# Kernel optimization log

Measured on AMD Instinct MI355X. Metric: run time of the kernel, lower is better.

The kernel has to match this reference:

```python
import jax, jax.numpy as jnp
import numpy as np

P_SIZE = 13
B_THRESH = 1.3  # |u| >= b -> hard 1.0
N_POW = 64      # u^n / (u^n + 1)


def make_dct_weight(p):
    idx = np.arange(p)
    Ci = np.where(idx == 0, 1.0 / np.sqrt(2.0), 1.0)
    cos = np.cos((2 * idx[:, None] + 1) * idx[None, :] * np.pi / (2 * p)) * Ci[None, :]  # [x,i]
    P = (2.0 / p) * np.einsum('xi,yj->xyij', cos, cos).reshape(p * p, p * p)
    return P.T.astype(np.float32).reshape(p * p, 1, p, p)


def conv2d(x, w, padding):
    return jax.lax.conv_general_dilated(x, w, (1, 1), padding,
                                        dimension_numbers=('NCHW', 'OIHW', 'NCHW'))


def udiff(u):
    # x^64/(x^64+1), saturated to 1 for |x| >= 1.3 (even power, sign-safe)
    au = jnp.abs(u)
    us = jnp.where(au < B_THRESH, u, 0.0)  # avoid overflow in pow
    y = us ** N_POW
    return jnp.where(au >= B_THRESH, jnp.ones_like(u), y / (y + 1.0))


def setup_inputs() -> dict:
    key = jax.random.key(0)
    k1, _ = jax.random.split(key)
    x = jax.random.uniform(k1, (2, 1, 512, 512), dtype=jnp.float32)
    sigma = jnp.full((1,), 0.1, dtype=jnp.float32)
    W_dct = jnp.asarray(make_dct_weight(P_SIZE))  # [p^2, 1, p, p], learnable in original
    return {"x": x, "sigma": sigma, "W_dct": W_dct}


def reference(x, sigma, W_dct):
    N, _, H, W = x.shape
    p = W_dct.shape[-1]
    pp = p * p
    # patch DCT: [N, p^2, H-p+1, W-p+1]
    t = conv2d(x, W_dct, 'VALID')
    nz = udiff(t / (3.0 * sigma))
    y = t * nz
    w = 1.0 / (1.0 + jnp.sum(nz, axis=1, keepdims=True))  # [N,1,H',W']
    # inverse transform as 1x1 conv with inv(dct matrix)
    Minv = jnp.linalg.inv(W_dct.reshape(pp, pp))
    z = jnp.einsum('kc,nchw->nkhw', Minv, y)
    z = w * z
    # overlap-add fold == conv with spatially-flipped identity patch kernel, full padding
    fold_k = jnp.flip(jnp.eye(pp, dtype=x.dtype).reshape(pp, p, p), axis=(1, 2))[None]  # [1,p^2,p,p]
    folded = conv2d(z, fold_k, [(p - 1, p - 1), (p - 1, p - 1)])  # [N,1,H,W]
    out = folded[:, :, p - 1:H - (p - 1), p - 1:W - (p - 1)]
    divisor = conv2d(w, jnp.ones((1, 1, p, p), x.dtype), 'VALID')
    return out / divisor
```

## Files before the change

### kernel.cpp

```cpp
#include <hip/hip_runtime.h>
#include <math.h>


#define P13    13
#define IMGW   512
#define OUTW   488
#define SEGH   31
#define NSEG   16
#define HCOLS  512
#define HPITCH 16

struct C1mat { float v[P13 * P13]; };

constexpr double kPI = 3.14159265358979323846264338327950288;

constexpr double ccos_pm_pi(double th) {
    double term = 1.0, s = 1.0;
    const double th2 = th * th;
    for (int n = 1; n <= 25; ++n) {
        term *= -th2 / (double)((2 * n - 1) * (2 * n));
        s += term;
    }
    return s;
}
constexpr double csqrt(double v) {
    double x = (v > 1.0) ? v : 1.0;
    for (int i = 0; i < 64; ++i) x = 0.5 * (x + v / x);
    return x;
}
constexpr C1mat make_c1() {
    C1mat m{};
    const double s213 = csqrt(2.0 / 13.0);
    const double is2  = 1.0 / csqrt(2.0);
    for (int x = 0; x < P13; ++x)
        for (int k = 0; k < P13; ++k) {
            int mm = ((2 * x + 1) * k) % 52;
            double th = (mm <= 26) ? (mm * kPI / 26.0) : ((mm - 52) * kPI / 26.0);
            double Ci = (k == 0) ? is2 : 1.0;
            m.v[x * P13 + k] = (float)(s213 * Ci * ccos_pm_pi(th));
        }
    return m;
}
__device__ constexpr C1mat c1c = make_c1();

struct CTab { int idx[P13][P13]; bool neg[P13][P13]; float a[14]; float b[6]; };
constexpr CTab make_ctab() {
    CTab t{};
    const double s213 = csqrt(2.0 / 13.0);
    for (int q = 0; q <= 12; ++q) t.a[q] = (float)(s213 * ccos_pm_pi(q * kPI / 26.0));
    t.a[13] = (float)(s213 / csqrt(2.0));
    for (int q = 0; q < 6; ++q) t.b[q] = (float)(2.0 * ccos_pm_pi((q + 1) * kPI / 13.0));
    for (int r = 0; r < P13; ++r)
        for (int c = 0; c < P13; ++c) {
            if (c == 0) { t.idx[r][c] = 13; t.neg[r][c] = false; continue; }
            int m = ((2 * r + 1) * c) % 52;
            int q; bool n;
            if (m <= 13)      { q = m;      n = false; }
            else if (m <= 26) { q = 26 - m; n = true;  }
            else if (m <= 39) { q = m - 26; n = true;  }
            else              { q = 52 - m; n = false; }
            t.idx[r][c] = q; t.neg[r][c] = n;
        }
    return t;
}
constexpr CTab ctab = make_ctab();

#define KC(r, c) (ctab.neg[(r)][(c)] ? -As[ctab.idx[(r)][(c)]] : As[ctab.idx[(r)][(c)]])

struct FalseT { static constexpr bool value = false; };
struct TrueT  { static constexpr bool value = true; };

#define ROR16_ADD(v, N)                                                        \
    v += __int_as_float(__builtin_amdgcn_mov_dpp(__float_as_int(v),            \
                                                 0x120 + (N), 0xF, 0xF, true))

__device__ __forceinline__ void fold_vert(const float (&tn)[P13], const float (&As)[14],
                                          float w1, float (&H)[P13])
{
#pragma unroll
    for (int dx = 0; dx < 6; ++dx) {
        float E = KC(dx, 0) * tn[0];
#pragma unroll
        for (int i = 2; i < P13; i += 2) E = fmaf(KC(dx, i), tn[i], E);
        float O = KC(dx, 1) * tn[1];
#pragma unroll
        for (int i = 3; i < P13; i += 2) O = fmaf(KC(dx, i), tn[i], O);
        H[dx]      = fmaf(w1, E + O, H[dx]);
        H[12 - dx] = fmaf(w1, E - O, H[12 - dx]);
    }
    float z6 = KC(6, 0) * tn[0];
#pragma unroll
    for (int i = 2; i < P13; i += 2) z6 = fmaf(KC(6, i), tn[i], z6);
    H[6] = fmaf(w1, z6, H[6]);
}

__global__ __launch_bounds__(256) void dct2net_k2(
    const float* __restrict__ xg, const float* __restrict__ sigmag,
    float* __restrict__ Hg, float* __restrict__ Wg)
{
    __shared__ float c1lds[169];
    const int tid = threadIdx.x;
    if (tid < 169) c1lds[tid] = c1c.v[tid];
    __syncthreads();

    const int lane = tid & 63;
    const int wv   = tid >> 6;
    const int g    = lane >> 4;
    const int jj   = lane & 15;
    const int img  = blockIdx.z;
    const int hs   = blockIdx.y * SEGH;
    const int segrows = (OUTW - hs < SEGH) ? (OUTW - hs) : SEGH;
    const int cbw  = blockIdx.x * 16 + wv * 4;
    const int col  = cbw + g;

    const float inv3s = 1.0f / (3.0f * sigmag[0]);
    const float* xin  = xg + (size_t)img * IMGW * IMGW;

    float As[14], Bs[6];
#pragma unroll
    for (int q = 0; q < 14; ++q) As[q] = ctab.a[q];
#pragma unroll
    for (int q = 0; q < 6; ++q) Bs[q] = ctab.b[q];
#pragma unroll
    for (int q = 0; q < 14; ++q) asm("" : "+s"(As[q]));
#pragma unroll
    for (int q = 0; q < 6; ++q) asm("" : "+s"(Bs[q]));

    float c1col[P13];
#pragma unroll
    for (int y = 0; y < P13; ++y)
        c1col[y] = (jj < 13) ? c1lds[y * P13 + jj] * inv3s : 0.0f;

    float T0[P13], T1[P13], dr[P13], Hr[P13], wr[12], Rv[P13];
#pragma unroll
    for (int k = 0; k < P13; ++k) { T0[k]=0; T1[k]=0; dr[k]=0; Hr[k]=0; Rv[k]=0; }
#pragma unroll
    for (int k = 0; k < 12; ++k) wr[k] = 0.0f;
    float vs = 0.0f, Rprev = 0.0f;

    int xcol = cbw + (lane & 15); xcol = (xcol < IMGW - 1) ? xcol : (IMGW - 1);
    const float* xp    = xin + (size_t)hs * IMGW;
    const float* xlast = xin + (size_t)(IMGW - 1) * IMGW;
    float xv = xp[xcol];
    xp += IMGW;

    float* Hp = Hg + ((size_t)img * OUTW + hs) * HCOLS * HPITCH;
    float* Wp = Wg + ((size_t)img * IMGW + hs) * IMGW;
    const int voH = col * HPITCH + jj;
    const int voW = col;

    auto front = [&]() -> float {
        float xw[P13];
#pragma unroll
        for (int y = 0; y < P13; ++y)
            xw[y] = __int_as_float(
                __builtin_amdgcn_ds_bpermute(4 * (g + y), __float_as_int(xv)));
        { const float* xq = (xp < xlast) ? xp : xlast; xv = xq[xcol]; xp += IMGW; }
        float a0 = c1col[0] * xw[0], a1 = c1col[1] * xw[1];
#pragma unroll
        for (int y = 2; y < P13; y += 2) a0 = fmaf(c1col[y], xw[y], a0);
#pragma unroll
        for (int y = 3; y < P13; y += 2) a1 = fmaf(c1col[y], xw[y], a1);
        return a0 + a1;
    };
    auto pushRv = [&](float Rn) {
#pragma unroll
        for (int q = 0; q < P13 - 1; ++q) Rv[q] = Rv[q + 1];
        Rv[P13 - 1] = Rn;
    };
    auto pushd = [&](float Rn) {
        float dn = Rn - Rprev; Rprev = Rn;
#pragma unroll
        for (int q = 0; q < P13 - 1; ++q) dr[q] = dr[q + 1];
        dr[P13 - 1] = dn;
    };
    auto matvec = [&](float (&T)[P13]) {
        float Se[6], So[6];
#pragma unroll
        for (int k = 0; k < 6; ++k) { Se[k] = Rv[k] + Rv[12 - k]; So[k] = Rv[k] - Rv[12 - k]; }
#pragma unroll
        for (int i = 0; i < P13; ++i) {
            float t;
            if ((i & 1) == 0) {
                t = KC(6, i) * Rv[6];
#pragma unroll
                for (int k = 0; k < 6; ++k) t = fmaf(KC(k, i), Se[k], t);
            } else {
                t = KC(0, i) * So[0];
#pragma unroll
                for (int k = 1; k < 6; ++k) t = fmaf(KC(k, i), So[k], t);
            }
            T[i] = t;
        }
    };
    auto sf = [&](const float (&T)[P13], bool rt) {
        float tn[P13]; float pnzr = 0.0f;
#pragma unroll
        for (int i = 0; i < P13; ++i) {
            float p2 = fminf(T[i] * T[i], 1.69f);
            float p4 = p2 * p2, p8 = p4 * p4, p16 = p8 * p8, p32 = p16 * p16, p64 = p32 * p32;
            float r  = __builtin_amdgcn_rcpf(p64 + 1.0f);
            pnzr += r;
            tn[i] = fmaf(-T[i], r, T[i]);
        }
        float pnz = 13.0f - pnzr;
        ROR16_ADD(pnz, 1); ROR16_ADD(pnz, 2); ROR16_ADD(pnz, 4); ROR16_ADD(pnz, 8);
        const float w = __builtin_amdgcn_rcpf(1.0f + pnz);
        vs += w;
        fold_vert(tn, As, w, Hr);
        if (rt) {
            Hp[voH] = Hr[0];
            Hp += HCOLS * HPITCH;
            if (jj == 0) Wp[voW] = vs;
            Wp += IMGW;
            vs -= wr[0];
        }
#pragma unroll
        for (int q = 0; q < 11; ++q) wr[q] = wr[q + 1];
        wr[11] = w;
#pragma unroll
        for (int q = 0; q < P13 - 1; ++q) Hr[q] = Hr[q + 1];
        Hr[P13 - 1] = 0.0f;
    };
    auto recur = [&](auto INTOT0, bool rt) {
        float Rn = front();
        float dn = Rn - Rprev; Rprev = Rn;
        float dl = dr[0];
#pragma unroll
        for (int q = 0; q < P13 - 1; ++q) dr[q] = dr[q + 1];
        dr[P13 - 1] = dn;
        float Pe = dn - dl, Po = dn + dl;
#pragma unroll
        for (int i = 0; i < P13; ++i) {
            float tp2 = decltype(INTOT0)::value ? T0[i] : T1[i];
            float tp1 = decltype(INTOT0)::value ? T1[i] : T0[i];
            float c2 = (i == 0) ? 2.0f : ((i <= 6) ? Bs[i - 1] : -Bs[12 - i]);
            float t = fmaf(c2, tp1, -tp2);
            float kc = (i == 0) ? As[13] : As[i];
            t = (i & 1) ? fmaf(-kc, Po, t) : fmaf(kc, Pe, t);
            if constexpr (decltype(INTOT0)::value) T0[i] = t; else T1[i] = t;
        }
        if constexpr (decltype(INTOT0)::value) sf(T0, rt); else sf(T1, rt);
    };

    { float Rn = front(); Rprev = Rn; pushRv(Rn); }
#pragma unroll 1
    for (int k = 1; k < 12; ++k) { float Rn = front(); pushd(Rn); pushRv(Rn); }
    { float Rn = front(); pushd(Rn); pushRv(Rn); matvec(T0); sf(T0, false); }
    { float Rn = front(); pushd(Rn); pushRv(Rn); matvec(T1); sf(T1, false); }
    {
        int ks = 0; const int S = 10 + segrows;
#pragma unroll 1
        while (ks + 2 <= S) {
            recur(TrueT{},  ks     >= 10);
            recur(FalseT{}, ks + 1 >= 10);
            ks += 2;
        }
        if (ks < S) recur(TrueT{}, ks >= 10);
    }
}

__global__ __launch_bounds__(256) void dct2net_k3(
    const float* __restrict__ Hg, const float* __restrict__ Wg,
    const float* __restrict__ sigmag, float* __restrict__ outg)
{
    __shared__ float U[4][76][14];
    __shared__ float vw[4][80];
    const int tid  = threadIdx.x;
    const int lane = tid & 63;
    const int wv   = tid >> 6;
    const int img  = blockIdx.z;
    const int a0   = blockIdx.y * 4;
    const int a    = a0 + wv;
    const int cb   = blockIdx.x * 64;

    const float t3s = 3.0f * sigmag[0];

    float As[14];
#pragma unroll
    for (int q = 0; q < 14; ++q) As[q] = ctab.a[q];
#pragma unroll
    for (int q = 0; q < 14; ++q) asm("" : "+s"(As[q]));

    int c = cb + lane; c = (c < 499) ? c : 499;
    const float* hp = &Hg[(((size_t)img * OUTW + a) * HCOLS + c) * HPITCH];
    float4 m0 = *(const float4*)hp;
    float4 m1 = *(const float4*)(hp + 4);
    float4 m2 = *(const float4*)(hp + 8);
    float  m3 = hp[12];
    float  wm = Wg[((size_t)img * IMGW + a) * IMGW + c];

    const bool halo = (tid < 48);
    const int  hr = tid / 12;
    const int  hm = tid - hr * 12;
    float4 s0 = {0,0,0,0}, s1 = {0,0,0,0}, s2 = {0,0,0,0};
    float  s3 = 0.0f, ws = 0.0f;
    if (halo) {
        const int ah = a0 + hr;
        int c2 = cb + 64 + hm; c2 = (c2 < 499) ? c2 : 499;
        const float* hq = &Hg[(((size_t)img * OUTW + ah) * HCOLS + c2) * HPITCH];
        s0 = *(const float4*)hq;
        s1 = *(const float4*)(hq + 4);
        s2 = *(const float4*)(hq + 8);
        s3 = hq[12];
        ws = Wg[((size_t)img * IMGW + ah) * IMGW + c2];
    }

    auto buildU = [&](const float (&hv)[P13], int uw, int uli) {
#pragma unroll
        for (int dy = 0; dy < 6; ++dy) {
            float e = KC(dy, 0) * hv[0];
#pragma unroll
            for (int j = 2; j < P13; j += 2) e = fmaf(KC(dy, j), hv[j], e);
            float o = KC(dy, 1) * hv[1];
#pragma unroll
            for (int j = 3; j < P13; j += 2) o = fmaf(KC(dy, j), hv[j], o);
            U[uw][uli][dy]      = e + o;
            U[uw][uli][12 - dy] = e - o;
        }
        float gsum = ((hv[4] - hv[2]) + (hv[8] - hv[6])) + (hv[12] - hv[10]);
        U[uw][uli][6] = fmaf(As[0], gsum, As[13] * hv[0]);
    };

    {
        float hv[P13] = {m0.x,m0.y,m0.z,m0.w, m1.x,m1.y,m1.z,m1.w,
                         m2.x,m2.y,m2.z,m2.w, m3};
        buildU(hv, wv, lane);
        vw[wv][lane] = wm;
    }
    if (halo) {
        float hv[P13] = {s0.x,s0.y,s0.z,s0.w, s1.x,s1.y,s1.z,s1.w,
                         s2.x,s2.y,s2.z,s2.w, s3};
        buildU(hv, hr, 64 + hm);
        vw[hr][64 + hm] = ws;
    }
    __syncthreads();

    float num = 0.0f;
#pragma unroll
    for (int dy = 0; dy < P13; ++dy) num += U[wv][lane + 12 - dy][dy];
    float den = 0.0f;
#pragma unroll
    for (int d = 0; d < P13; ++d) den += vw[wv][lane + d];
    const int ow = cb + lane;
    if (ow < OUTW)
        outg[((size_t)img * OUTW + a) * OUTW + ow] =
            num * t3s * __builtin_amdgcn_rcpf(den);
}

extern "C" void kernel_launch(void* const* d_in, const int* in_sizes, int n_in,
                              void* d_out, int out_size, void* d_ws, size_t ws_size,
                              hipStream_t stream)
{
    const float* x     = (const float*)d_in[0];
    const float* sigma = (const float*)d_in[1];
    float* out = (float*)d_out;

    float* Hg = (float*)d_ws;
    float* Wg = Hg + (size_t)2 * OUTW * HCOLS * HPITCH;

    dct2net_k2<<<dim3(32, NSEG, 2), 256, 0, stream>>>(x, sigma, Hg, Wg);
    dct2net_k3<<<dim3(8, 122, 2), 256, 0, stream>>>(Hg, Wg, sigma, out);
}
```

Before: 180.6 us.

## Stage input window in LDS and transpose intermediate H to column-major planes

In the first kernel, the 13 ds_bpermute cross-lane shuffles per row are replaced by a small per-group LDS window that is read back with four float4 loads. The row loads are double-buffered across two registers, and the coefficient column is pre-shifted per group. The intermediate H buffer changes from [row][col][16] to [row][16][col], so the per-lane stores in k2 and the per-coefficient loads in k3 become coalesced. The U LDS array is padded to width 15 to avoid bank conflicts. The LDS write/read ordering within a wave relies on lockstep execution without explicit barriers, which is a correctness risk.

```diff
diff --git a/kernel.cpp b/kernel.cpp
--- a/kernel.cpp
+++ b/kernel.cpp
@@ -99,6 +99,7 @@
     float* __restrict__ Hg, float* __restrict__ Wg)
 {
     __shared__ float c1lds[169];
+    __shared__ float xlds[4][4][20];
     const int tid = threadIdx.x;
     if (tid < 169) c1lds[tid] = c1c.v[tid];
     __syncthreads();
@@ -126,10 +127,15 @@
 #pragma unroll
     for (int q = 0; q < 6; ++q) asm("" : "+s"(Bs[q]));
 
-    float c1col[P13];
-#pragma unroll
-    for (int y = 0; y < P13; ++y)
-        c1col[y] = (jj < 13) ? c1lds[y * P13 + jj] * inv3s : 0.0f;
+    float c1x[16];
+#pragma unroll
+    for (int p = 0; p < 16; ++p) {
+        int y = p - g;
+        int yc = (y < 0) ? 0 : ((y > 12) ? 12 : y);
+        int jc = (jj < 13) ? jj : 0;
+        float v = c1lds[yc * 13 + jc];
+        c1x[p] = (y >= 0 && y < 13 && jj < 13) ? v * inv3s : 0.0f;
+    }
 
     float T0[P13], T1[P13], dr[P13], Hr[P13], wr[12], Rv[P13];
 #pragma unroll
@@ -139,28 +145,37 @@
     float vs = 0.0f, Rprev = 0.0f;
 
     int xcol = cbw + (lane & 15); xcol = (xcol < IMGW - 1) ? xcol : (IMGW - 1);
-    const float* xp    = xin + (size_t)hs * IMGW;
     const float* xlast = xin + (size_t)(IMGW - 1) * IMGW;
-    float xv = xp[xcol];
-    xp += IMGW;
-
-    float* Hp = Hg + ((size_t)img * OUTW + hs) * HCOLS * HPITCH;
+
+    float xvA, xvB;
+    {
+        const float* r0 = xin + (size_t)hs * IMGW;
+        float t0 = r0[xcol];
+        xlds[wv][g][jj] = t0;
+        const float* r1 = xin + (size_t)(hs + 1) * IMGW;
+        xvA = r1[xcol];
+    }
+    const float* xp = xin + (size_t)(hs + 2) * IMGW;
+
+    float* Hp = Hg + ((size_t)img * OUTW + hs) * HPITCH * HCOLS;
     float* Wp = Wg + ((size_t)img * IMGW + hs) * IMGW;
-    const int voH = col * HPITCH + jj;
+    const int voH = jj * HCOLS + col;
     const int voW = col;
 
-    auto front = [&]() -> float {
-        float xw[P13];
-#pragma unroll
-        for (int y = 0; y < P13; ++y)
-            xw[y] = __int_as_float(
-                __builtin_amdgcn_ds_bpermute(4 * (g + y), __float_as_int(xv)));
-        { const float* xq = (xp < xlast) ? xp : xlast; xv = xq[xcol]; xp += IMGW; }
-        float a0 = c1col[0] * xw[0], a1 = c1col[1] * xw[1];
-#pragma unroll
-        for (int y = 2; y < P13; y += 2) a0 = fmaf(c1col[y], xw[y], a0);
-#pragma unroll
-        for (int y = 3; y < P13; y += 2) a1 = fmaf(c1col[y], xw[y], a1);
+    auto front = [&](float& xvW, float& xvL) -> float {
+        float4 q0 = *(const float4*)&xlds[wv][g][0];
+        float4 q1 = *(const float4*)&xlds[wv][g][4];
+        float4 q2 = *(const float4*)&xlds[wv][g][8];
+        float4 q3 = *(const float4*)&xlds[wv][g][12];
+        { const float* xq = (xp < xlast) ? xp : xlast; xvL = xq[xcol]; xp += IMGW; }
+        xlds[wv][g][jj] = xvW;
+        float xq_[16] = {q0.x,q0.y,q0.z,q0.w, q1.x,q1.y,q1.z,q1.w,
+                         q2.x,q2.y,q2.z,q2.w, q3.x,q3.y,q3.z,q3.w};
+        float a0 = c1x[0] * xq_[0], a1 = c1x[1] * xq_[1];
+#pragma unroll
+        for (int p = 2; p < 16; p += 2) a0 = fmaf(c1x[p], xq_[p], a0);
+#pragma unroll
+        for (int p = 3; p < 16; p += 2) a1 = fmaf(c1x[p], xq_[p], a1);
         return a0 + a1;
     };
     auto pushRv = [&](float Rn) {
@@ -210,7 +225,7 @@
         fold_vert(tn, As, w, Hr);
         if (rt) {
             Hp[voH] = Hr[0];
-            Hp += HCOLS * HPITCH;
+            Hp += HPITCH * HCOLS;
             if (jj == 0) Wp[voW] = vs;
             Wp += IMGW;
             vs -= wr[0];
@@ -222,8 +237,8 @@
         for (int q = 0; q < P13 - 1; ++q) Hr[q] = Hr[q + 1];
         Hr[P13 - 1] = 0.0f;
     };
-    auto recur = [&](auto INTOT0, bool rt) {
-        float Rn = front();
+    auto recur = [&](auto INTOT0, float& xvW, float& xvL, bool rt) {
+        float Rn = front(xvW, xvL);
         float dn = Rn - Rprev; Rprev = Rn;
         float dl = dr[0];
 #pragma unroll
@@ -243,20 +258,24 @@
         if constexpr (decltype(INTOT0)::value) sf(T0, rt); else sf(T1, rt);
     };
 
-    { float Rn = front(); Rprev = Rn; pushRv(Rn); }
+    { float Rn = front(xvA, xvB); Rprev = Rn; pushRv(Rn); }
+    { float Rn = front(xvB, xvA); pushd(Rn); pushRv(Rn); }
 #pragma unroll 1
-    for (int k = 1; k < 12; ++k) { float Rn = front(); pushd(Rn); pushRv(Rn); }
-    { float Rn = front(); pushd(Rn); pushRv(Rn); matvec(T0); sf(T0, false); }
-    { float Rn = front(); pushd(Rn); pushRv(Rn); matvec(T1); sf(T1, false); }
+    for (int k = 2; k < 12; k += 2) {
+        float Rn = front(xvA, xvB); pushd(Rn); pushRv(Rn);
+        float Rm = front(xvB, xvA); pushd(Rm); pushRv(Rm);
+    }
+    { float Rn = front(xvA, xvB); pushd(Rn); pushRv(Rn); matvec(T0); sf(T0, false); }
+    { float Rn = front(xvB, xvA); pushd(Rn); pushRv(Rn); matvec(T1); sf(T1, false); }
     {
         int ks = 0; const int S = 10 + segrows;
 #pragma unroll 1
         while (ks + 2 <= S) {
-            recur(TrueT{},  ks     >= 10);
-            recur(FalseT{}, ks + 1 >= 10);
+            recur(TrueT{},  xvA, xvB, ks     >= 10);
+            recur(FalseT{}, xvB, xvA, ks + 1 >= 10);
             ks += 2;
         }
-        if (ks < S) recur(TrueT{}, ks >= 10);
+        if (ks < S) recur(TrueT{}, xvA, xvB, ks >= 10);
     }
 }
 
@@ -264,7 +283,7 @@
     const float* __restrict__ Hg, const float* __restrict__ Wg,
     const float* __restrict__ sigmag, float* __restrict__ outg)
 {
-    __shared__ float U[4][76][14];
+    __shared__ float U[4][76][15];
     __shared__ float vw[4][80];
     const int tid  = threadIdx.x;
     const int lane = tid & 63;
@@ -283,55 +302,47 @@
     for (int q = 0; q < 14; ++q) asm("" : "+s"(As[q]));
 
     int c = cb + lane; c = (c < 499) ? c : 499;
-    const float* hp = &Hg[(((size_t)img * OUTW + a) * HCOLS + c) * HPITCH];
-    float4 m0 = *(const float4*)hp;
-    float4 m1 = *(const float4*)(hp + 4);
-    float4 m2 = *(const float4*)(hp + 8);
-    float  m3 = hp[12];
-    float  wm = Wg[((size_t)img * IMGW + a) * IMGW + c];
+    const float* hb = Hg + ((size_t)img * OUTW + a) * HPITCH * HCOLS + c;
+    float hv[P13];
+#pragma unroll
+    for (int j = 0; j < P13; ++j) hv[j] = hb[j * HCOLS];
+    float wm = Wg[((size_t)img * IMGW + a) * IMGW + c];
 
     const bool halo = (tid < 48);
     const int  hr = tid / 12;
     const int  hm = tid - hr * 12;
-    float4 s0 = {0,0,0,0}, s1 = {0,0,0,0}, s2 = {0,0,0,0};
-    float  s3 = 0.0f, ws = 0.0f;
+    float sv[P13]; float ws = 0.0f;
+#pragma unroll
+    for (int j = 0; j < P13; ++j) sv[j] = 0.0f;
     if (halo) {
         const int ah = a0 + hr;
         int c2 = cb + 64 + hm; c2 = (c2 < 499) ? c2 : 499;
-        const float* hq = &Hg[(((size_t)img * OUTW + ah) * HCOLS + c2) * HPITCH];
-        s0 = *(const float4*)hq;
-        s1 = *(const float4*)(hq + 4);
-        s2 = *(const float4*)(hq + 8);
-        s3 = hq[12];
+        const float* hq = Hg + ((size_t)img * OUTW + ah) * HPITCH * HCOLS + c2;
+#pragma unroll
+        for (int j = 0; j < P13; ++j) sv[j] = hq[j * HCOLS];
         ws = Wg[((size_t)img * IMGW + ah) * IMGW + c2];
     }
 
-    auto buildU = [&](const float (&hv)[P13], int uw, int uli) {
+    auto buildU = [&](const float (&h)[P13], int uw, int uli) {
 #pragma unroll
         for (int dy = 0; dy < 6; ++dy) {
-            float e = KC(dy, 0) * hv[0];
-#pragma unroll
-            for (int j = 2; j < P13; j += 2) e = fmaf(KC(dy, j), hv[j], e);
-            float o = KC(dy, 1) * hv[1];
-#pragma unroll
-            for (int j = 3; j < P13; j += 2) o = fmaf(KC(dy, j), hv[j], o);
+            float e = KC(dy, 0) * h[0];
+#pragma unroll
+            for (int j = 2; j < P13; j += 2) e = fmaf(KC(dy, j), h[j], e);
+            float o = KC(dy, 1) * h[1];
+#pragma unroll
+            for (int j = 3; j < P13; j += 2) o = fmaf(KC(dy, j), h[j], o);
             U[uw][uli][dy]      = e + o;
             U[uw][uli][12 - dy] = e - o;
         }
-        float gsum = ((hv[4] - hv[2]) + (hv[8] - hv[6])) + (hv[12] - hv[10]);
-        U[uw][uli][6] = fmaf(As[0], gsum, As[13] * hv[0]);
-    };
-
-    {
-        float hv[P13] = {m0.x,m0.y,m0.z,m0.w, m1.x,m1.y,m1.z,m1.w,
-                         m2.x,m2.y,m2.z,m2.w, m3};
-        buildU(hv, wv, lane);
-        vw[wv][lane] = wm;
-    }
+        float gsum = ((h[4] - h[2]) + (h[8] - h[6])) + (h[12] - h[10]);
+        U[uw][uli][6] = fmaf(As[0], gsum, As[13] * h[0]);
+    };
+
+    buildU(hv, wv, lane);
+    vw[wv][lane] = wm;
     if (halo) {
-        float hv[P13] = {s0.x,s0.y,s0.z,s0.w, s1.x,s1.y,s1.z,s1.w,
-                         s2.x,s2.y,s2.z,s2.w, s3};
-        buildU(hv, hr, 64 + hm);
+        buildU(sv, hr, 64 + hm);
         vw[hr][64 + hm] = ws;
     }
     __syncthreads();
@@ -357,7 +368,7 @@
     float* out = (float*)d_out;
 
     float* Hg = (float*)d_ws;
-    float* Wg = Hg + (size_t)2 * OUTW * HCOLS * HPITCH;
+    float* Wg = Hg + (size_t)2 * OUTW * HPITCH * HCOLS;
 
     dct2net_k2<<<dim3(32, NSEG, 2), 256, 0, stream>>>(x, sigma, Hg, Wg);
     dct2net_k3<<<dim3(8, 122, 2), 256, 0, stream>>>(Hg, Wg, sigma, out);
```

New measurement: 176.7 us. -2.2%, faster.
